# Performance work log

Hardware: AMD Instinct MI355X
Metric: run time of the kernel (lower is better)

## Reference

```python
import jax, jax.numpy as jnp
import numpy as np

SD = 4          # spixel_downsize
EPS = 1e-5      # BatchNorm eps
SLOPE = 0.01    # nn.LeakyReLU() default negative_slope


def deconv3d(x, w, stride, pad):
    # w is in torch ConvTranspose3d layout: (in_ch, out_ch, kd, kh, kw).
    # Transposed conv == conv with lhs_dilation=stride, flipped kernel,
    # padding (k-1-p) per spatial dim.
    kd, kh, kw = w.shape[2], w.shape[3], w.shape[4]
    wc = jnp.transpose(jnp.flip(w, axis=(2, 3, 4)), (1, 0, 2, 3, 4))  # OIDHW
    pads = [(kd - 1 - pad[0],) * 2, (kh - 1 - pad[1],) * 2, (kw - 1 - pad[2],) * 2]
    return jax.lax.conv_general_dilated(
        x, wc, window_strides=(1, 1, 1), padding=pads,
        lhs_dilation=(stride, stride, stride),
        dimension_numbers=('NCDHW', 'OIDHW', 'NCDHW'))


def bn_lrelu(x, g, b, relu=True):
    # inference BatchNorm3d with running_mean=0, running_var=1 (fresh BN)
    scale = (g / jnp.sqrt(1.0 + EPS)).reshape(1, -1, 1, 1, 1)
    y = x * scale + b.reshape(1, -1, 1, 1, 1)
    return jax.nn.leaky_relu(y, SLOPE) if relu else y


def _sl(s):
    # shift s in {+1, 0, -1} -> (agg slice, cost slice) along one spatial dim
    if s == 1:
        return slice(SD, None), slice(None, -SD)
    if s == 0:
        return slice(None), slice(None)
    return slice(None, -SD), slice(SD, None)


def setup_inputs() -> dict:
    key = jax.random.key(0)
    ks = jax.random.split(key, 8)
    b, d, h, w = 1, 24, 64, 128
    f32 = jnp.float32
    cv1 = jax.random.normal(ks[0], (b, 32, d, h, w), f32)                 # cv[-1]
    cv0 = jax.random.normal(ks[1], (b, 16, 2 * d, 2 * h, 2 * w), f32)     # cv[-2]
    sp = jax.random.uniform(ks[2], (b, 9, 4 * h, 4 * w), f32)             # superpixel probs
    w0a = jax.random.normal(ks[3], (32, 32, 3, 1, 1), f32) * 0.05
    w0b = jax.random.normal(ks[4], (32, 16, 4, 2, 2), f32) * 0.05
    w1a = jax.random.normal(ks[5], (32, 16, 3, 1, 1), f32) * 0.05
    w1b = jax.random.normal(ks[6], (16, 1, 4, 2, 2), f32) * 0.05
    g0, g1, g2, g3 = (jnp.ones((c,), f32) for c in (32, 16, 16, 1))
    b0, b1, b2, b3 = (jnp.zeros((c,), f32) for c in (32, 16, 16, 1))
    return dict(cv1=cv1, cv0=cv0, sp=sp, w0a=w0a, w0b=w0b, w1a=w1a, w1b=w1b,
                g0=g0, g1=g1, g2=g2, g3=g3, b0=b0, b1=b1, b2=b2, b3=b3)


def reference(cv1, cv0, sp, w0a, w0b, w1a, w1b, g0, g1, g2, g3, b0, b1, b2, b3):
    # conv[0]: BasicConv(32->32, k(3,1,1), s1, p(1,0,0)) + BasicConv(32->16, k(4,2,2), s2, p(1,0,0))
    x = bn_lrelu(deconv3d(cv1, w0a, 1, (1, 0, 0)), g0, b0)
    x = bn_lrelu(deconv3d(x, w0b, 2, (1, 0, 0)), g1, b1)
    x = jnp.concatenate((x, cv0), axis=1)
    # conv[1] (sp==2 branch): 32->16 then 16->out_dim, bn=relu=bnrelu=True
    x = bn_lrelu(deconv3d(x, w1a, 1, (1, 0, 0)), g2, b2)
    cost = bn_lrelu(deconv3d(x, w1b, 2, (1, 0, 0)), g3, b3)  # (b, 1, 4d, 4h, 4w)

    sp5 = sp[:, None]  # (b, 1, 9, H, W)
    agg = jnp.zeros_like(cost)
    k = 0
    for hy in (1, 0, -1):        # 9 fixed superpixel-neighbor shifts
        ah, ch = _sl(hy)
        for wx in (1, 0, -1):
            aw, cw = _sl(wx)
            wgt = sp5[:, :, k, ah, aw][:, :, None]  # (b,1,1,H',W')
            agg = agg.at[:, :, :, ah, aw].add(cost[:, :, :, ch, cw] * wgt)
            k += 1
    return agg
```

## Files before the change

### kernel.cpp

```cpp
#include <hip/hip_runtime.h>
#include <hip/hip_bf16.h>

typedef __hip_bfloat16 bf16;

constexpr int cD0 = 24,  cH0 = 64,  cW0 = 128;
constexpr int cD1 = 48,  cH1 = 128, cW1 = 256;
constexpr int cD2 = 96,  cH2 = 256, cW2 = 512;
constexpr size_t PL0 = (size_t)cD0 * cH0 * cW0;
constexpr size_t PL1 = (size_t)cD1 * cH1 * cW1;
constexpr size_t PL2 = (size_t)cD2 * cH2 * cW2;

__device__ __forceinline__ float b2f(bf16 v) { return __bfloat162float(v); }
__device__ __forceinline__ bf16  f2b(float v) { return __float2bfloat16(v); }
__device__ __forceinline__ float lrelu(float v) { return v >= 0.f ? v : 0.01f * v; }
__device__ __forceinline__ float us2f(ushort u) { return __uint_as_float(((uint)u) << 16); }
__device__ __forceinline__ ushort f2us(float v) { return __bfloat16_as_ushort(f2b(v)); }

__global__ __launch_bounds__(256) void kW(const float* __restrict__ w0a,
                                          const float* __restrict__ w0b,
                                          const float* __restrict__ w1a,
                                          const float* __restrict__ w1b,
                                          float* __restrict__ wA,
                                          float* __restrict__ wB,
                                          float* __restrict__ wD,
                                          float* __restrict__ wE) {
    const int tid = threadIdx.x;
    for (int i = tid; i < 3072; i += 256) {
        int ci = i / 96, r = i - ci * 96, co = r / 3, u = r - co * 3;
        wA[(u * 32 + ci) * 32 + co] = w0a[i];
    }
    for (int i = tid; i < 8192; i += 256) {
        int ci = i >> 8, co = (i >> 4) & 15, kd = (i >> 2) & 3, kh = (i >> 1) & 1, kw = i & 1;
        wB[(((kd * 2 + kh) * 32 + ci) * 2 + kw) * 16 + co] = w0b[i];
    }
    for (int i = tid; i < 1536; i += 256) {
        int ci = i / 48, r = i - ci * 48, co = r / 3, u = r - co * 3;
        wD[(u * 32 + ci) * 16 + co] = w1a[i];
    }
    {
        int i = tid;
        int ci = i >> 4, kd = (i >> 2) & 3, kh = (i >> 1) & 1, kw = i & 1;
        wE[(kd * 4 + kh * 2 + kw) * 16 + ci] = w1b[i];
    }
}

__global__ __launch_bounds__(256) void kA(const float* __restrict__ cv1,
                                          const float* __restrict__ wA,
                                          const float* __restrict__ g0,
                                          const float* __restrict__ b0,
                                          bf16* __restrict__ x1) {
    const int pos = blockIdx.x * 256 + threadIdx.x;
    const int x = pos & (cW0 - 1);
    const int y = (pos >> 7) & (cH0 - 1);
    const int z = pos >> 13;

    float acc[32] = {};

    #pragma unroll
    for (int u = 0; u < 3; ++u) {
        const int zi = z + 1 - u;
        if (zi < 0 || zi >= cD0) continue;
        const float* src = cv1 + (size_t)(zi * cH0 + y) * cW0 + x;
        float v[32];
        #pragma unroll
        for (int ci = 0; ci < 32; ++ci) v[ci] = src[ci * PL0];
        #pragma unroll
        for (int ci = 0; ci < 32; ++ci) {
            const float* w = wA + (u * 32 + ci) * 32;
            #pragma unroll
            for (int q = 0; q < 32; ++q) acc[q] += v[ci] * w[q];
        }
    }
    #pragma unroll
    for (int co = 0; co < 32; ++co) {
        const float sc = g0[co] * (1.0f / sqrtf(1.0f + 1e-5f));
        const float bi = b0[co];
        x1[co * PL0 + (size_t)(z * cH0 + y) * cW0 + x] = f2b(lrelu(acc[co] * sc + bi));
    }
}

__global__ __launch_bounds__(256) void kB(const bf16* __restrict__ x1,
                                          const float* __restrict__ wB,
                                          const float* __restrict__ g1,
                                          const float* __restrict__ b1,
                                          bf16* __restrict__ x2) {
    const int lane = threadIdx.x & 63;
    const int wv   = __builtin_amdgcn_readfirstlane(threadIdx.x >> 6);
    const int b_   = blockIdx.x;
    const int oh = b_ & 127;
    const int od = (b_ >> 7) * 4 + wv;
    const int ih = oh >> 1, kh = oh & 1;
    const int p  = (od + 1) & 1;
    const int iw0 = 2 * lane;

    float acc[4][16] = {};

    #pragma unroll
    for (int j = 0; j < 2; ++j) {
        const int kd = p + 2 * j;
        const int id = (od + 1 - kd) >> 1;
        if (id < 0 || id >= cD0) continue;
        const bf16* src = x1 + (size_t)(id * cH0 + ih) * cW0 + iw0;
        uint px[32];
        #pragma unroll
        for (int ci = 0; ci < 32; ++ci) px[ci] = *(const uint*)(src + ci * PL0);
        const float* wkd = wB + (size_t)((kd * 2 + kh) * 32) * 32;
        #pragma unroll
        for (int ci = 0; ci < 32; ++ci) {
            const float v0 = us2f((ushort)(px[ci] & 0xffffu));
            const float v1 = us2f((ushort)(px[ci] >> 16));
            const float* w0 = wkd + ci * 32;
            const float* w1 = w0 + 16;
            #pragma unroll
            for (int q = 0; q < 16; ++q) {
                acc[0][q] += v0 * w0[q];
                acc[1][q] += v0 * w1[q];
                acc[2][q] += v1 * w0[q];
                acc[3][q] += v1 * w1[q];
            }
        }
    }
    const size_t obase = (size_t)(od * cH1 + oh) * cW1 + 4 * lane;
    #pragma unroll
    for (int co = 0; co < 16; ++co) {
        const float sc = g1[co] * (1.0f / sqrtf(1.0f + 1e-5f));
        const float bi = b1[co];
        ushort4 s;
        s.x = f2us(lrelu(acc[0][co] * sc + bi));
        s.y = f2us(lrelu(acc[1][co] * sc + bi));
        s.z = f2us(lrelu(acc[2][co] * sc + bi));
        s.w = f2us(lrelu(acc[3][co] * sc + bi));
        *(ushort4*)(x2 + co * PL1 + obase) = s;
    }
}

__global__ __launch_bounds__(256) void kD(const bf16* __restrict__ x2,
                                          const float* __restrict__ cv0,
                                          const float* __restrict__ wD,
                                          const float* __restrict__ g2,
                                          const float* __restrict__ b2v,
                                          bf16* __restrict__ x3) {
    const int bid = blockIdx.x;
    const int b_  = (bid & 7) * 192 + (bid >> 3);
    const int zq = b_ % 12;
    const int y  = b_ / 12;
    const int lane = threadIdx.x & 63;
    const int wv   = __builtin_amdgcn_readfirstlane(threadIdx.x >> 6);
    const int z  = zq * 4 + wv;
    const int x0 = 4 * lane;

    float acc[4][16] = {};

    #pragma unroll
    for (int u = 0; u < 3; ++u) {
        const int zi = z + 1 - u;
        if (zi < 0 || zi >= cD1) continue;
        const size_t base = (size_t)(zi * cH1 + y) * cW1 + x0;
        {
            ushort4 px[16];
            #pragma unroll
            for (int ci = 0; ci < 16; ++ci) px[ci] = *(const ushort4*)(x2 + ci * PL1 + base);
            #pragma unroll
            for (int ci = 0; ci < 16; ++ci) {
                const float v0 = us2f(px[ci].x), v1 = us2f(px[ci].y);
                const float v2 = us2f(px[ci].z), v3 = us2f(px[ci].w);
                const float* w = wD + (u * 32 + ci) * 16;
                #pragma unroll
                for (int q = 0; q < 16; ++q) {
                    acc[0][q] += v0 * w[q]; acc[1][q] += v1 * w[q];
                    acc[2][q] += v2 * w[q]; acc[3][q] += v3 * w[q];
                }
            }
        }
        {
            float4 pc[16];
            #pragma unroll
            for (int ci = 0; ci < 16; ++ci) pc[ci] = *(const float4*)(cv0 + ci * PL1 + base);
            #pragma unroll
            for (int ci = 0; ci < 16; ++ci) {
                const float* w = wD + (u * 32 + 16 + ci) * 16;
                #pragma unroll
                for (int q = 0; q < 16; ++q) {
                    acc[0][q] += pc[ci].x * w[q]; acc[1][q] += pc[ci].y * w[q];
                    acc[2][q] += pc[ci].z * w[q]; acc[3][q] += pc[ci].w * w[q];
                }
            }
        }
    }
    const size_t obase = (size_t)(z * cH1 + y) * cW1 + x0;
    #pragma unroll
    for (int co = 0; co < 16; ++co) {
        const float sc = g2[co] * (1.0f / sqrtf(1.0f + 1e-5f));
        const float bi = b2v[co];
        ushort4 s;
        s.x = f2us(lrelu(acc[0][co] * sc + bi));
        s.y = f2us(lrelu(acc[1][co] * sc + bi));
        s.z = f2us(lrelu(acc[2][co] * sc + bi));
        s.w = f2us(lrelu(acc[3][co] * sc + bi));
        *(ushort4*)(x3 + co * PL1 + obase) = s;
    }
}

__global__ __launch_bounds__(256) void kE(const bf16* __restrict__ x3,
                                          const float* __restrict__ wE,
                                          const float* __restrict__ g3,
                                          const float* __restrict__ b3v,
                                          bf16* __restrict__ cost) {
    const int lane = threadIdx.x & 63;
    const int wv   = __builtin_amdgcn_readfirstlane(threadIdx.x >> 6);
    const int b_   = blockIdx.x;
    const int iwp = lane + 64 * (b_ & 1);
    const int ih  = (b_ >> 1) & 127;
    const int od  = (b_ >> 8) * 4 + wv;
    const int p   = (od + 1) & 1;
    const int iw0 = 2 * iwp;

    float a[2][2][2] = {};
    #pragma unroll
    for (int j = 0; j < 2; ++j) {
        const int kd = p + 2 * j;
        const int id = (od + 1 - kd) >> 1;
        if (id < 0 || id >= cD1) continue;
        const size_t base = (size_t)(id * cH1 + ih) * cW1 + iw0;
        uint px[16];
        #pragma unroll
        for (int ci = 0; ci < 16; ++ci) px[ci] = *(const uint*)(x3 + ci * PL1 + base);
        const float* w = wE + kd * 64;
        #pragma unroll
        for (int ci = 0; ci < 16; ++ci) {
            const float v0 = us2f((ushort)(px[ci] & 0xffffu));
            const float v1 = us2f((ushort)(px[ci] >> 16));
            a[0][0][0] += v0 * w[ci];      a[0][0][1] += v0 * w[16 + ci];
            a[0][1][0] += v0 * w[32 + ci]; a[0][1][1] += v0 * w[48 + ci];
            a[1][0][0] += v1 * w[ci];      a[1][0][1] += v1 * w[16 + ci];
            a[1][1][0] += v1 * w[32 + ci]; a[1][1][1] += v1 * w[48 + ci];
        }
    }
    const float sc = g3[0] * (1.0f / sqrtf(1.0f + 1e-5f));
    const float bi = b3v[0];
    const size_t ob = (size_t)(od * cH2 + 2 * ih) * cW2 + 4 * iwp;
    ushort4 s;
    s.x = f2us(lrelu(a[0][0][0] * sc + bi));
    s.y = f2us(lrelu(a[0][0][1] * sc + bi));
    s.z = f2us(lrelu(a[1][0][0] * sc + bi));
    s.w = f2us(lrelu(a[1][0][1] * sc + bi));
    *(ushort4*)(cost + ob) = s;
    s.x = f2us(lrelu(a[0][1][0] * sc + bi));
    s.y = f2us(lrelu(a[0][1][1] * sc + bi));
    s.z = f2us(lrelu(a[1][1][0] * sc + bi));
    s.w = f2us(lrelu(a[1][1][1] * sc + bi));
    *(ushort4*)(cost + ob + cW2) = s;
}

__global__ __launch_bounds__(256) void kF(const bf16* __restrict__ cost,
                                          const float* __restrict__ sp,
                                          float* __restrict__ out) {
    const int t    = blockIdx.x * 256 + threadIdx.x;
    const int lane = t & 63;
    const int rowq = t >> 6;
    const int x0 = 4 * (lane + 64 * (rowq & 1));
    const int y  = (rowq >> 1) & 255;
    const int d0 = (rowq >> 9) * 4;
    const size_t plane = (size_t)cH2 * cW2;

    float4 wq[9];
    int cyc[3], cxc[3];
    #pragma unroll
    for (int r = 0; r < 3; ++r) {
        const int cy = y - 4 * (1 - r);
        const bool vy = (cy >= 0) && (cy < cH2);
        cyc[r] = vy ? cy : 0;
        #pragma unroll
        for (int c = 0; c < 3; ++c) {
            const int cx = x0 - 4 * (1 - c);
            const bool vx = (cx >= 0) && (cx < cW2);
            if (r == 0) cxc[c] = vx ? cx : 0;
            if (vy && vx)
                wq[r*3+c] = *(const float4*)(sp + (size_t)(r*3+c) * plane + (size_t)y * cW2 + x0);
            else
                wq[r*3+c] = make_float4(0.f, 0.f, 0.f, 0.f);
        }
    }
    #pragma unroll
    for (int dd = 0; dd < 4; ++dd) {
        const int d = d0 + dd;
        const bf16* cp = cost + (size_t)d * plane;
        float ax = 0.f, ay = 0.f, az = 0.f, aw = 0.f;
        #pragma unroll
        for (int r = 0; r < 3; ++r) {
            const bf16* rp = cp + (size_t)cyc[r] * cW2;
            #pragma unroll
            for (int c = 0; c < 3; ++c) {
                const ushort4 u = *(const ushort4*)(rp + cxc[c]);
                const float4 w = wq[r*3+c];
                ax += w.x * us2f(u.x); ay += w.y * us2f(u.y);
                az += w.z * us2f(u.z); aw += w.w * us2f(u.w);
            }
        }
        float4 o; o.x = ax; o.y = ay; o.z = az; o.w = aw;
        *(float4*)(out + (size_t)d * plane + (size_t)y * cW2 + x0) = o;
    }
}

extern "C" void kernel_launch(void* const* d_in, const int* in_sizes, int n_in,
                              void* d_out, int out_size, void* d_ws, size_t ws_size,
                              hipStream_t stream) {
    const float* cv1 = (const float*)d_in[0];
    const float* cv0 = (const float*)d_in[1];
    const float* sp  = (const float*)d_in[2];
    const float* w0a = (const float*)d_in[3];
    const float* w0b = (const float*)d_in[4];
    const float* w1a = (const float*)d_in[5];
    const float* w1b = (const float*)d_in[6];
    const float* g0  = (const float*)d_in[7];
    const float* g1  = (const float*)d_in[8];
    const float* g2  = (const float*)d_in[9];
    const float* g3  = (const float*)d_in[10];
    const float* b0  = (const float*)d_in[11];
    const float* b1  = (const float*)d_in[12];
    const float* b2  = (const float*)d_in[13];
    const float* b3  = (const float*)d_in[14];

    char* ws = (char*)d_ws;
    bf16* x1   = (bf16*)(ws);
    bf16* x2   = (bf16*)(ws + 12582912);
    bf16* x3   = (bf16*)(ws + 62914560);
    bf16* cost = (bf16*)(ws);

    float* wbase = (float*)((char*)d_out + 50331648 - 65536);
    float* wA = wbase;
    float* wB = wbase + 3072;
    float* wD = wbase + 3072 + 8192;
    float* wE = wD + 1536;

    kW<<<1,    256, 0, stream>>>(w0a, w0b, w1a, w1b, wA, wB, wD, wE);
    kA<<<768,  256, 0, stream>>>(cv1, wA, g0, b0, x1);
    kB<<<1536, 256, 0, stream>>>(x1, wB, g1, b1, x2);
    kD<<<1536, 256, 0, stream>>>(x2, cv0, wD, g2, b2, x3);
    kE<<<6144, 256, 0, stream>>>(x3, wE, g3, b3, cost);
    kF<<<3072, 256, 0, stream>>>(cost, sp, (float*)d_out);
}
```

Measured before the change: 439.4 us.

## Stage conv weights in LDS for kA/kE and remap kB block indexing

kA and kE now load their weights (and BN scale/bias for kA) straight into shared memory per block instead of reading a host-prepared global copy, which removes two of the weight transforms from the setup kernel. kA drops the 32-register input-vector preload and streams one channel at a time with float4 LDS weight reads, cutting register pressure. kB's block-to-output mapping is changed so the four waves in a block work on adjacent input rows at the same depth, which should improve locality of x1 reads. kE loads x3 per channel rather than preloading all 16 channels. The cost is per-block LDS fills and a barrier, plus less memory-level parallelism from issuing loads one at a time.

```diff
diff --git a/kernel.cpp b/kernel.cpp
--- a/kernel.cpp
+++ b/kernel.cpp
@@ -16,19 +16,11 @@
 __device__ __forceinline__ float us2f(ushort u) { return __uint_as_float(((uint)u) << 16); }
 __device__ __forceinline__ ushort f2us(float v) { return __bfloat16_as_ushort(f2b(v)); }
 
-__global__ __launch_bounds__(256) void kW(const float* __restrict__ w0a,
-                                          const float* __restrict__ w0b,
+__global__ __launch_bounds__(256) void kW(const float* __restrict__ w0b,
                                           const float* __restrict__ w1a,
-                                          const float* __restrict__ w1b,
-                                          float* __restrict__ wA,
                                           float* __restrict__ wB,
-                                          float* __restrict__ wD,
-                                          float* __restrict__ wE) {
+                                          float* __restrict__ wD) {
     const int tid = threadIdx.x;
-    for (int i = tid; i < 3072; i += 256) {
-        int ci = i / 96, r = i - ci * 96, co = r / 3, u = r - co * 3;
-        wA[(u * 32 + ci) * 32 + co] = w0a[i];
-    }
     for (int i = tid; i < 8192; i += 256) {
         int ci = i >> 8, co = (i >> 4) & 15, kd = (i >> 2) & 3, kh = (i >> 1) & 1, kw = i & 1;
         wB[(((kd * 2 + kh) * 32 + ci) * 2 + kw) * 16 + co] = w0b[i];
@@ -37,46 +29,55 @@
         int ci = i / 48, r = i - ci * 48, co = r / 3, u = r - co * 3;
         wD[(u * 32 + ci) * 16 + co] = w1a[i];
     }
-    {
-        int i = tid;
-        int ci = i >> 4, kd = (i >> 2) & 3, kh = (i >> 1) & 1, kw = i & 1;
-        wE[(kd * 4 + kh * 2 + kw) * 16 + ci] = w1b[i];
-    }
 }
 
 __global__ __launch_bounds__(256) void kA(const float* __restrict__ cv1,
-                                          const float* __restrict__ wA,
+                                          const float* __restrict__ w0a,
                                           const float* __restrict__ g0,
                                           const float* __restrict__ b0,
                                           bf16* __restrict__ x1) {
-    const int pos = blockIdx.x * 256 + threadIdx.x;
+    __shared__ float lw[3][32][32];
+    __shared__ float lsc[32], lbi[32];
+    const int tid = threadIdx.x;
+    for (int i = tid; i < 32 * 32 * 3; i += 256) {
+        int ci = i / 96, r = i - ci * 96, co = r / 3, u = r - co * 3;
+        lw[u][ci][co] = w0a[i];
+    }
+    if (tid < 32) {
+        lsc[tid] = g0[tid] * (1.0f / sqrtf(1.0f + 1e-5f));
+        lbi[tid] = b0[tid];
+    }
+    __syncthreads();
+
+    const int pos = blockIdx.x * 256 + tid;
     const int x = pos & (cW0 - 1);
     const int y = (pos >> 7) & (cH0 - 1);
     const int z = pos >> 13;
 
-    float acc[32] = {};
+    float acc[32];
+    #pragma unroll
+    for (int co = 0; co < 32; ++co) acc[co] = 0.f;
 
     #pragma unroll
     for (int u = 0; u < 3; ++u) {
         const int zi = z + 1 - u;
         if (zi < 0 || zi >= cD0) continue;
         const float* src = cv1 + (size_t)(zi * cH0 + y) * cW0 + x;
-        float v[32];
-        #pragma unroll
-        for (int ci = 0; ci < 32; ++ci) v[ci] = src[ci * PL0];
-        #pragma unroll
         for (int ci = 0; ci < 32; ++ci) {
-            const float* w = wA + (u * 32 + ci) * 32;
-            #pragma unroll
-            for (int q = 0; q < 32; ++q) acc[q] += v[ci] * w[q];
-        }
-    }
-    #pragma unroll
-    for (int co = 0; co < 32; ++co) {
-        const float sc = g0[co] * (1.0f / sqrtf(1.0f + 1e-5f));
-        const float bi = b0[co];
-        x1[co * PL0 + (size_t)(z * cH0 + y) * cW0 + x] = f2b(lrelu(acc[co] * sc + bi));
-    }
+            const float v = src[ci * PL0];
+            const float4* wp = (const float4*)&lw[u][ci][0];
+            #pragma unroll
+            for (int q = 0; q < 8; ++q) {
+                float4 wv = wp[q];
+                acc[4*q+0] += v * wv.x; acc[4*q+1] += v * wv.y;
+                acc[4*q+2] += v * wv.z; acc[4*q+3] += v * wv.w;
+            }
+        }
+    }
+    #pragma unroll
+    for (int co = 0; co < 32; ++co)
+        x1[co * PL0 + (size_t)(z * cH0 + y) * cW0 + x] =
+            f2b(lrelu(acc[co] * lsc[co] + lbi[co]));
 }
 
 __global__ __launch_bounds__(256) void kB(const bf16* __restrict__ x1,
@@ -87,11 +88,14 @@
     const int lane = threadIdx.x & 63;
     const int wv   = __builtin_amdgcn_readfirstlane(threadIdx.x >> 6);
     const int b_   = blockIdx.x;
-    const int oh = b_ & 127;
-    const int od = (b_ >> 7) * 4 + wv;
-    const int ih = oh >> 1, kh = oh & 1;
-    const int p  = (od + 1) & 1;
-    const int iw0 = 2 * lane;
+    const int s_   = b_ & 1;
+    const int ohq  = (b_ >> 1) & 15;
+    const int od   = b_ >> 5;
+    const int oh   = ohq * 8 + 2 * wv + s_;
+    const int ih   = ohq * 4 + wv;
+    const int kh   = s_;
+    const int p    = (od + 1) & 1;
+    const int iw0  = 2 * lane;
 
     float acc[4][16] = {};
 
@@ -202,16 +206,22 @@
 }
 
 __global__ __launch_bounds__(256) void kE(const bf16* __restrict__ x3,
-                                          const float* __restrict__ wE,
+                                          const float* __restrict__ w1b,
                                           const float* __restrict__ g3,
                                           const float* __restrict__ b3v,
                                           bf16* __restrict__ cost) {
-    const int lane = threadIdx.x & 63;
-    const int wv   = __builtin_amdgcn_readfirstlane(threadIdx.x >> 6);
-    const int b_   = blockIdx.x;
+    __shared__ float lw[256];
+    const int tid = threadIdx.x;
+    lw[tid] = w1b[tid];
+    __syncthreads();
+
+    const int t    = blockIdx.x * 256 + tid;
+    const int lane = t & 63;
+    const int wv_  = (t >> 6) & 3;
+    const int b_   = t >> 8;
     const int iwp = lane + 64 * (b_ & 1);
     const int ih  = (b_ >> 1) & 127;
-    const int od  = (b_ >> 8) * 4 + wv;
+    const int od  = (b_ >> 8) * 4 + wv_;
     const int p   = (od + 1) & 1;
     const int iw0 = 2 * iwp;
 
@@ -222,18 +232,16 @@
         const int id = (od + 1 - kd) >> 1;
         if (id < 0 || id >= cD1) continue;
         const size_t base = (size_t)(id * cH1 + ih) * cW1 + iw0;
-        uint px[16];
-        #pragma unroll
-        for (int ci = 0; ci < 16; ++ci) px[ci] = *(const uint*)(x3 + ci * PL1 + base);
-        const float* w = wE + kd * 64;
         #pragma unroll
         for (int ci = 0; ci < 16; ++ci) {
-            const float v0 = us2f((ushort)(px[ci] & 0xffffu));
-            const float v1 = us2f((ushort)(px[ci] >> 16));
-            a[0][0][0] += v0 * w[ci];      a[0][0][1] += v0 * w[16 + ci];
-            a[0][1][0] += v0 * w[32 + ci]; a[0][1][1] += v0 * w[48 + ci];
-            a[1][0][0] += v1 * w[ci];      a[1][0][1] += v1 * w[16 + ci];
-            a[1][1][0] += v1 * w[32 + ci]; a[1][1][1] += v1 * w[48 + ci];
+            const uint pk = *(const uint*)(x3 + ci * PL1 + base);
+            const float v0 = us2f((ushort)(pk & 0xffffu));
+            const float v1 = us2f((ushort)(pk >> 16));
+            const float* w = &lw[ci * 16 + kd * 4];
+            a[0][0][0] += v0 * w[0]; a[0][0][1] += v0 * w[1];
+            a[0][1][0] += v0 * w[2]; a[0][1][1] += v0 * w[3];
+            a[1][0][0] += v1 * w[0]; a[1][0][1] += v1 * w[1];
+            a[1][1][0] += v1 * w[2]; a[1][1][1] += v1 * w[3];
         }
     }
     const float sc = g3[0] * (1.0f / sqrtf(1.0f + 1e-5f));
@@ -328,15 +336,13 @@
     bf16* cost = (bf16*)(ws);
 
     float* wbase = (float*)((char*)d_out + 50331648 - 65536);
-    float* wA = wbase;
-    float* wB = wbase + 3072;
-    float* wD = wbase + 3072 + 8192;
-    float* wE = wD + 1536;
-
-    kW<<<1,    256, 0, stream>>>(w0a, w0b, w1a, w1b, wA, wB, wD, wE);
-    kA<<<768,  256, 0, stream>>>(cv1, wA, g0, b0, x1);
+    float* wB = wbase;
+    float* wD = wbase + 8192;
+
+    kW<<<1,    256, 0, stream>>>(w0b, w1a, wB, wD);
+    kA<<<768,  256, 0, stream>>>(cv1, w0a, g0, b0, x1);
     kB<<<1536, 256, 0, stream>>>(x1, wB, g1, b1, x2);
     kD<<<1536, 256, 0, stream>>>(x2, cv0, wD, g2, b2, x3);
-    kE<<<6144, 256, 0, stream>>>(x3, wE, g3, b3, cost);
+    kE<<<6144, 256, 0, stream>>>(x3, w1b, g3, b3, cost);
     kF<<<3072, 256, 0, stream>>>(cost, sp, (float*)d_out);
 }
```

New measurement: 590.9 us. 1.34x slower.
